# Performance work log

Measured on AMD Instinct MI355X. Metric: run time of the kernel, lower is better.

Reference implementation:

```python
import jax, jax.numpy as jnp
import numpy as np

N = 100000
E = 1600000
D_IN = 64
D_OUT = 64


def setup_inputs() -> dict:
    key = jax.random.key(0)
    k1, k2, k3, k4 = jax.random.split(key, 4)
    x = jax.random.normal(k1, (N, D_IN), dtype=jnp.float32)
    edge_index = jax.random.randint(k2, (2, E), 0, N, dtype=jnp.int32)
    # nn.Linear(in, out): weight [out, in]; we store W as [in, out] for x @ W
    W = jax.random.normal(k3, (D_IN, D_OUT), dtype=jnp.float32) * (1.0 / np.sqrt(D_IN))
    b = jax.random.normal(k4, (D_OUT,), dtype=jnp.float32) * 0.01
    return {"x": x, "edge_index": edge_index, "W": W, "b": b}


def reference(x, edge_index, W, b):
    n = x.shape[0]
    src, tgt = edge_index[0], edge_index[1]
    # gather neighbor feats and scatter-add into source nodes: agg[src] += x[tgt]
    agg = jax.ops.segment_sum(x[tgt], src, num_segments=n)  # [N, D_in]
    # degree normalization: bincount(src) + eps
    counts = jax.ops.segment_sum(jnp.ones((src.shape[0],), dtype=x.dtype), src,
                                 num_segments=n) + 1e-6  # [N]
    agg = agg / counts[:, None]
    return agg @ W + b  # [N, D_out]
```

## Files before the change

### kernel.cpp

```cpp
#include <hip/hip_runtime.h>
#include <hip/hip_fp16.h>

#define D 64
#define NPB 32
#define LOGNPB 5
#define BCAPS 128
#define NSHARD 8
#define FCHUNK 8192
#define STAGECAP 1024
#define SORTCAP 1280

typedef int v4i __attribute__((ext_vector_type(4)));

__device__ __forceinline__ float bcast(float v, int k) {
    return __uint_as_float(__builtin_amdgcn_readlane(__float_as_uint(v), k));
}

__global__ __launch_bounds__(256, 2) void fused_partition_gemm(
    const int* __restrict__ src, const int* __restrict__ tgt,
    int* __restrict__ gcur, int* __restrict__ part,
    const float* __restrict__ x, const float* __restrict__ W,
    __half* __restrict__ y,
    int E, int nbuck, int fill_blocks, int N, int gemm_nwaves)
{
    extern __shared__ int hist[];
    int tid = threadIdx.x;

    if ((int)blockIdx.x < fill_blocks) {
        int xsh = blockIdx.x & (NSHARD - 1);
        int* mycur  = gcur + (size_t)xsh * nbuck;
        int* mypart = part + (size_t)xsh * nbuck * BCAPS;

        for (int i = tid; i < nbuck; i += 256) hist[i] = 0;
        __syncthreads();

        int base = blockIdx.x * FCHUNK;
        int end = base + FCHUNK < E ? base + FCHUNK : E;
        int nfull = (end - base) & ~7;

        for (int i = base + tid * 8; i + 8 <= end; i += 256 * 8) {
            v4i s0 = __builtin_nontemporal_load((const v4i*)(src + i));
            v4i s1 = __builtin_nontemporal_load((const v4i*)(src + i + 4));
            int ss[8] = {s0.x, s0.y, s0.z, s0.w, s1.x, s1.y, s1.z, s1.w};
            #pragma unroll
            for (int j = 0; j < 8; ++j)
                atomicAdd(&hist[ss[j] >> LOGNPB], 1);
        }
        for (int i = base + nfull + tid; i < end; i += 256)
            atomicAdd(&hist[src[i] >> LOGNPB], 1);
        __syncthreads();

        for (int bkt = tid; bkt < nbuck; bkt += 256) {
            int h = hist[bkt];
            hist[bkt] = h ? atomicAdd(&mycur[bkt], h) : 0;
        }
        __syncthreads();

        for (int i = base + tid * 8; i + 8 <= end; i += 256 * 8) {
            v4i s0 = *(const v4i*)(src + i);
            v4i s1 = *(const v4i*)(src + i + 4);
            v4i t0 = *(const v4i*)(tgt + i);
            v4i t1 = *(const v4i*)(tgt + i + 4);
            int ss[8] = {s0.x, s0.y, s0.z, s0.w, s1.x, s1.y, s1.z, s1.w};
            int tt[8] = {t0.x, t0.y, t0.z, t0.w, t1.x, t1.y, t1.z, t1.w};
            int pos[8], bk[8];
            #pragma unroll
            for (int j = 0; j < 8; ++j) {
                bk[j] = ss[j] >> LOGNPB;
                pos[j] = atomicAdd(&hist[bk[j]], 1);
            }
            #pragma unroll
            for (int j = 0; j < 8; ++j)
                if ((unsigned)pos[j] < BCAPS)
                    mypart[(unsigned)(bk[j] * BCAPS + pos[j])] =
                        ((ss[j] & (NPB - 1)) << 20) | tt[j];
        }
        for (int i = base + nfull + tid; i < end; i += 256) {
            int s = src[i], t = tgt[i];
            int b = s >> LOGNPB;
            int p = atomicAdd(&hist[b], 1);
            if ((unsigned)p < BCAPS)
                mypart[(unsigned)(b * BCAPS + p)] = ((s & (NPB - 1)) << 20) | t;
        }
    } else {
        int lane = tid & 63;
        if ((int)blockIdx.x == fill_blocks && tid < D)
            y[(unsigned)(N * D + tid)] = __float2half(0.0f);

        float wcol[D];
        #pragma unroll
        for (int k = 0; k < D; ++k)
            wcol[k] = W[k * D + lane];

        int gw = ((int)blockIdx.x - fill_blocks) * 4 + (tid >> 6);
        for (int n = gw * 4; n < N; n += gemm_nwaves * 4) {
            int i1 = n + 1 < N ? n + 1 : N - 1;
            int i2 = n + 2 < N ? n + 2 : N - 1;
            int i3 = n + 3 < N ? n + 3 : N - 1;
            float x0 = x[((unsigned)n  << 6) | lane];
            float x1 = x[((unsigned)i1 << 6) | lane];
            float x2 = x[((unsigned)i2 << 6) | lane];
            float x3 = x[((unsigned)i3 << 6) | lane];

            float o0 = 0, o1 = 0, o2 = 0, o3 = 0;
            #pragma unroll
            for (int k = 0; k < D; ++k) {
                float w = wcol[k];
                o0 += bcast(x0, k) * w;
                o1 += bcast(x1, k) * w;
                o2 += bcast(x2, k) * w;
                o3 += bcast(x3, k) * w;
            }
            y[((unsigned)n << 6) | lane] = __float2half(o0);
            if (n + 1 < N) y[((unsigned)(n + 1) << 6) | lane] = __float2half(o1);
            if (n + 2 < N) y[((unsigned)(n + 2) << 6) | lane] = __float2half(o2);
            if (n + 3 < N) y[((unsigned)(n + 3) << 6) | lane] = __float2half(o3);
        }
    }
}

__global__ __launch_bounds__(256) void bucket_gather(
    const __half* __restrict__ y, const int* __restrict__ gcur,
    const int* __restrict__ part, const float* __restrict__ bias_v,
    float* __restrict__ out, int N, int nbuck, int zrow)
{
    __shared__ int cnt_s[NPB];
    __shared__ int off_s[NPB];
    __shared__ int cur_s[NPB];
    __shared__ int segc[NSHARD];
    __shared__ int segoff[NSHARD + 1];
    __shared__ int stage[STAGECAP];
    __shared__ __align__(16) int sortbuf[SORTCAP];
    int tid = threadIdx.x, wave = tid >> 6, lane = tid & 63;
    int bk = blockIdx.x;

    if (tid < NPB) cnt_s[tid] = 0;
    if (tid < NSHARD) {
        int c = gcur[(size_t)tid * nbuck + bk];
        segc[tid] = c > BCAPS ? BCAPS : c;
    }
    for (int i = tid; i < SORTCAP; i += 256) sortbuf[i] = zrow;
    __syncthreads();

    if (tid == 0) {
        int acc = 0;
        #pragma unroll
        for (int sh = 0; sh < NSHARD; ++sh) { segoff[sh] = acc; acc += segc[sh]; }
        segoff[NSHARD] = acc;
    }
    __syncthreads();

    int half = tid >> 7;
    int hid  = tid & 127;

    #pragma unroll
    for (int sh = 0; sh < NSHARD; sh += 2) {
        int s2 = sh + half;
        int c = segc[s2];
        if (hid < c)
            stage[segoff[s2] + hid] =
                part[(unsigned)((s2 * nbuck + bk) * BCAPS + hid)];
    }
    __syncthreads();
    int tot = segoff[NSHARD];

    for (int i = tid; i < tot; i += 256)
        atomicAdd(&cnt_s[stage[i] >> 20], 1);
    __syncthreads();

    if (wave == 0) {
        int v = (lane < NPB) ? cnt_s[lane] : 0;
        int r = (v + 7) & ~7;
        int s = r;
        #pragma unroll
        for (int d = 1; d < NPB; d <<= 1) {
            int t = __shfl_up(s, d);
            if ((lane & (NPB - 1)) >= d) s += t;
        }
        if (lane < NPB) {
            off_s[lane] = s - r;
            cur_s[lane] = s - r;
        }
    }
    __syncthreads();

    for (int i = tid; i < tot; i += 256) {
        int w = stage[i];
        int p = atomicAdd(&cur_s[w >> 20], 1);
        if (p < SORTCAP) sortbuf[p] = w & 0xFFFFF;
    }
    __syncthreads();

    float bias = bias_v[lane];
    for (int r = wave; r < NPB; r += 4) {
        int n = (bk << LOGNPB) + r;
        if (n >= N) break;
        int dg = cnt_s[r];
        int rdeg = (dg + 7) & ~7;
        int start = off_s[r];

        float a0 = 0, a1 = 0, a2 = 0, a3 = 0, a4 = 0, a5 = 0, a6 = 0, a7 = 0;
        for (int i = start; i < start + rdeg; i += 8) {
            int4 q0 = *(const int4*)&sortbuf[i];
            int4 q1 = *(const int4*)&sortbuf[i + 4];
            a0 += __half2float(y[((unsigned)q0.x << 6) | lane]);
            a1 += __half2float(y[((unsigned)q0.y << 6) | lane]);
            a2 += __half2float(y[((unsigned)q0.z << 6) | lane]);
            a3 += __half2float(y[((unsigned)q0.w << 6) | lane]);
            a4 += __half2float(y[((unsigned)q1.x << 6) | lane]);
            a5 += __half2float(y[((unsigned)q1.y << 6) | lane]);
            a6 += __half2float(y[((unsigned)q1.z << 6) | lane]);
            a7 += __half2float(y[((unsigned)q1.w << 6) | lane]);
        }
        float scale = 1.0f / ((float)dg + 1e-6f);
        float a = ((a0 + a1) + (a2 + a3)) + ((a4 + a5) + (a6 + a7));
        __builtin_nontemporal_store(a * scale + bias,
                                    &out[((unsigned)n << 6) | lane]);
    }
}

extern "C" void kernel_launch(void* const* d_in, const int* in_sizes, int n_in,
                              void* d_out, int out_size, void* d_ws, size_t ws_size,
                              hipStream_t stream) {
    const float* x  = (const float*)d_in[0];
    const int*   ei = (const int*)d_in[1];
    const float* W  = (const float*)d_in[2];
    const float* b  = (const float*)d_in[3];
    float* out = (float*)d_out;

    int N = in_sizes[0] / D;
    int E = in_sizes[1] / 2;
    const int* src = ei;
    const int* tgt = ei + E;

    int nbuck = (N + NPB - 1) >> LOGNPB;

    int* gcur = (int*)d_ws;
    int* part = gcur + (size_t)NSHARD * nbuck;
    __half* y = (__half*)(part + (size_t)NSHARD * nbuck * BCAPS);

    hipMemsetAsync(gcur, 0, (size_t)NSHARD * nbuck * sizeof(int), stream);

    int fb = (E + FCHUNK - 1) / FCHUNK;
    const int gemm_blocks = 1024;
    fused_partition_gemm<<<fb + gemm_blocks, 256, nbuck * sizeof(int), stream>>>(
        src, tgt, gcur, part, x, W, y, E, nbuck, fb, N, gemm_blocks * 4);

    bucket_gather<<<nbuck, 256, 0, stream>>>(y, gcur, part, b, out, N, nbuck, N);
}
```

Measured before the change: 169.2 us.

## Replace sharded global-atomic bucket partition with per-block local prefix-sum layout

Each fill block now does a block-wide prefix scan over its bucket histogram and writes edges into its own contiguous chunk, recording a packed offset/count header per bucket. This removes the global atomics on shard cursors and the memset of those cursors. The gather kernel reads all fb headers per bucket, scans them, and binary-searches to pull edge words from many scattered segments. That adds fb header reads per bucket and a more fragmented part read, and it relies on fb≤256, per-thread bucket count ≤16 and per-chunk counts fitting in 14 bits.

```diff
diff --git a/kernel.cpp b/kernel.cpp
--- a/kernel.cpp
+++ b/kernel.cpp
@@ -4,9 +4,8 @@
 #define D 64
 #define NPB 32
 #define LOGNPB 5
-#define BCAPS 128
-#define NSHARD 8
 #define FCHUNK 8192
+#define FBMAX 256
 #define STAGECAP 1024
 #define SORTCAP 1280
 
@@ -18,23 +17,23 @@
 
 __global__ __launch_bounds__(256, 2) void fused_partition_gemm(
     const int* __restrict__ src, const int* __restrict__ tgt,
-    int* __restrict__ gcur, int* __restrict__ part,
+    int* __restrict__ hdr, int* __restrict__ part,
     const float* __restrict__ x, const float* __restrict__ W,
     __half* __restrict__ y,
     int E, int nbuck, int fill_blocks, int N, int gemm_nwaves)
 {
     extern __shared__ int hist[];
-    int tid = threadIdx.x;
+    __shared__ int wsum_s[4];
+    int tid = threadIdx.x, lane = tid & 63, wave = tid >> 6;
 
     if ((int)blockIdx.x < fill_blocks) {
-        int xsh = blockIdx.x & (NSHARD - 1);
-        int* mycur  = gcur + (size_t)xsh * nbuck;
-        int* mypart = part + (size_t)xsh * nbuck * BCAPS;
+        int b = blockIdx.x;
+        int* mypart = part + (size_t)b * FCHUNK;
 
         for (int i = tid; i < nbuck; i += 256) hist[i] = 0;
         __syncthreads();
 
-        int base = blockIdx.x * FCHUNK;
+        int base = b * FCHUNK;
         int end = base + FCHUNK < E ? base + FCHUNK : E;
         int nfull = (end - base) & ~7;
 
@@ -50,9 +49,33 @@
             atomicAdd(&hist[src[i] >> LOGNPB], 1);
         __syncthreads();
 
-        for (int bkt = tid; bkt < nbuck; bkt += 256) {
-            int h = hist[bkt];
-            hist[bkt] = h ? atomicAdd(&mycur[bkt], h) : 0;
+        int cpb = (nbuck + 255) >> 8;
+        int c[16];
+        int base_i = tid * cpb, tsum = 0;
+        for (int j = 0; j < cpb; ++j) {
+            int idx = base_i + j;
+            int v = (idx < nbuck) ? hist[idx] : 0;
+            c[j] = v; tsum += v;
+        }
+        int inc = tsum;
+        #pragma unroll
+        for (int d2 = 1; d2 < 64; d2 <<= 1) {
+            int t = __shfl_up(inc, d2);
+            if (lane >= d2) inc += t;
+        }
+        if (lane == 63) wsum_s[wave] = inc;
+        __syncthreads();
+        int wbase = 0;
+        for (int wv = 0; wv < wave; ++wv) wbase += wsum_s[wv];
+        int run = wbase + inc - tsum;
+        for (int j = 0; j < cpb; ++j) {
+            int idx = base_i + j;
+            if (idx < nbuck) {
+                hdr[(size_t)b * nbuck + idx] =
+                    (int)(((unsigned)run << 14) | (unsigned)c[j]);
+                hist[idx] = run;
+                run += c[j];
+            }
         }
         __syncthreads();
 
@@ -63,27 +86,20 @@
             v4i t1 = *(const v4i*)(tgt + i + 4);
             int ss[8] = {s0.x, s0.y, s0.z, s0.w, s1.x, s1.y, s1.z, s1.w};
             int tt[8] = {t0.x, t0.y, t0.z, t0.w, t1.x, t1.y, t1.z, t1.w};
-            int pos[8], bk[8];
-            #pragma unroll
-            for (int j = 0; j < 8; ++j) {
-                bk[j] = ss[j] >> LOGNPB;
-                pos[j] = atomicAdd(&hist[bk[j]], 1);
-            }
+            int pos[8];
             #pragma unroll
             for (int j = 0; j < 8; ++j)
-                if ((unsigned)pos[j] < BCAPS)
-                    mypart[(unsigned)(bk[j] * BCAPS + pos[j])] =
-                        ((ss[j] & (NPB - 1)) << 20) | tt[j];
+                pos[j] = atomicAdd(&hist[ss[j] >> LOGNPB], 1);
+            #pragma unroll
+            for (int j = 0; j < 8; ++j)
+                mypart[pos[j]] = ((ss[j] & (NPB - 1)) << 20) | tt[j];
         }
         for (int i = base + nfull + tid; i < end; i += 256) {
             int s = src[i], t = tgt[i];
-            int b = s >> LOGNPB;
-            int p = atomicAdd(&hist[b], 1);
-            if ((unsigned)p < BCAPS)
-                mypart[(unsigned)(b * BCAPS + p)] = ((s & (NPB - 1)) << 20) | t;
+            int p = atomicAdd(&hist[s >> LOGNPB], 1);
+            mypart[p] = ((s & (NPB - 1)) << 20) | t;
         }
     } else {
-        int lane = tid & 63;
         if ((int)blockIdx.x == fill_blocks && tid < D)
             y[(unsigned)(N * D + tid)] = __float2half(0.0f);
 
@@ -92,7 +108,7 @@
         for (int k = 0; k < D; ++k)
             wcol[k] = W[k * D + lane];
 
-        int gw = ((int)blockIdx.x - fill_blocks) * 4 + (tid >> 6);
+        int gw = ((int)blockIdx.x - fill_blocks) * 4 + wave;
         for (int n = gw * 4; n < N; n += gemm_nwaves * 4) {
             int i1 = n + 1 < N ? n + 1 : N - 1;
             int i2 = n + 2 < N ? n + 2 : N - 1;
@@ -120,49 +136,56 @@
 }
 
 __global__ __launch_bounds__(256) void bucket_gather(
-    const __half* __restrict__ y, const int* __restrict__ gcur,
+    const __half* __restrict__ y, const int* __restrict__ hdr,
     const int* __restrict__ part, const float* __restrict__ bias_v,
-    float* __restrict__ out, int N, int nbuck, int zrow)
+    float* __restrict__ out, int N, int nbuck, int fb, int zrow)
 {
+    __shared__ int goff_s[FBMAX];
+    __shared__ int soff_s[FBMAX];
+    __shared__ int wsum_s[4];
+    __shared__ int tot_s;
     __shared__ int cnt_s[NPB];
     __shared__ int off_s[NPB];
     __shared__ int cur_s[NPB];
-    __shared__ int segc[NSHARD];
-    __shared__ int segoff[NSHARD + 1];
     __shared__ int stage[STAGECAP];
     __shared__ __align__(16) int sortbuf[SORTCAP];
     int tid = threadIdx.x, wave = tid >> 6, lane = tid & 63;
     int bk = blockIdx.x;
 
+    int cb = 0;
+    if (tid < fb) {
+        unsigned h = (unsigned)hdr[(size_t)tid * nbuck + bk];
+        goff_s[tid] = (int)(h >> 14);
+        cb = (int)(h & 16383u);
+    }
+    int inc = cb;
+    #pragma unroll
+    for (int d2 = 1; d2 < 64; d2 <<= 1) {
+        int t = __shfl_up(inc, d2);
+        if (lane >= d2) inc += t;
+    }
+    if (lane == 63) wsum_s[wave] = inc;
     if (tid < NPB) cnt_s[tid] = 0;
-    if (tid < NSHARD) {
-        int c = gcur[(size_t)tid * nbuck + bk];
-        segc[tid] = c > BCAPS ? BCAPS : c;
-    }
     for (int i = tid; i < SORTCAP; i += 256) sortbuf[i] = zrow;
     __syncthreads();
-
-    if (tid == 0) {
-        int acc = 0;
-        #pragma unroll
-        for (int sh = 0; sh < NSHARD; ++sh) { segoff[sh] = acc; acc += segc[sh]; }
-        segoff[NSHARD] = acc;
-    }
-    __syncthreads();
-
-    int half = tid >> 7;
-    int hid  = tid & 127;
-
-    #pragma unroll
-    for (int sh = 0; sh < NSHARD; sh += 2) {
-        int s2 = sh + half;
-        int c = segc[s2];
-        if (hid < c)
-            stage[segoff[s2] + hid] =
-                part[(unsigned)((s2 * nbuck + bk) * BCAPS + hid)];
-    }
-    __syncthreads();
-    int tot = segoff[NSHARD];
+    int wbase = 0;
+    for (int wv = 0; wv < wave; ++wv) wbase += wsum_s[wv];
+    soff_s[tid] = wbase + inc - cb;
+    if (tid == 255) tot_s = wbase + inc;
+    __syncthreads();
+
+    int tot = tot_s;
+    if (tot > STAGECAP) tot = STAGECAP;
+
+    for (int i = tid; i < tot; i += 256) {
+        int lo = 0, hi = fb - 1;
+        while (lo < hi) {
+            int mid = (lo + hi + 1) >> 1;
+            if (soff_s[mid] <= i) lo = mid; else hi = mid - 1;
+        }
+        stage[i] = part[(size_t)lo * FCHUNK + goff_s[lo] + (i - soff_s[lo])];
+    }
+    __syncthreads();
 
     for (int i = tid; i < tot; i += 256)
         atomicAdd(&cnt_s[stage[i] >> 20], 1);
@@ -173,9 +196,9 @@
         int r = (v + 7) & ~7;
         int s = r;
         #pragma unroll
-        for (int d = 1; d < NPB; d <<= 1) {
-            int t = __shfl_up(s, d);
-            if ((lane & (NPB - 1)) >= d) s += t;
+        for (int d2 = 1; d2 < NPB; d2 <<= 1) {
+            int t = __shfl_up(s, d2);
+            if ((lane & (NPB - 1)) >= d2) s += t;
         }
         if (lane < NPB) {
             off_s[lane] = s - r;
@@ -234,17 +257,15 @@
     const int* tgt = ei + E;
 
     int nbuck = (N + NPB - 1) >> LOGNPB;
-
-    int* gcur = (int*)d_ws;
-    int* part = gcur + (size_t)NSHARD * nbuck;
-    __half* y = (__half*)(part + (size_t)NSHARD * nbuck * BCAPS);
-
-    hipMemsetAsync(gcur, 0, (size_t)NSHARD * nbuck * sizeof(int), stream);
-
     int fb = (E + FCHUNK - 1) / FCHUNK;
+
+    int* hdr = (int*)d_ws;
+    int* part = hdr + (size_t)fb * nbuck;
+    __half* y = (__half*)(part + (size_t)fb * FCHUNK);
+
     const int gemm_blocks = 1024;
     fused_partition_gemm<<<fb + gemm_blocks, 256, nbuck * sizeof(int), stream>>>(
-        src, tgt, gcur, part, x, W, y, E, nbuck, fb, N, gemm_blocks * 4);
-
-    bucket_gather<<<nbuck, 256, 0, stream>>>(y, gcur, part, b, out, N, nbuck, N);
-}
+        src, tgt, hdr, part, x, W, y, E, nbuck, fb, N, gemm_blocks * 4);
+
+    bucket_gather<<<nbuck, 256, 0, stream>>>(y, hdr, part, b, out, N, nbuck, fb, N);
+}
```

Result: slower. 180.7 us (+6.8%).
